# Kernel tuning notes

Hardware: AMD Instinct MI355X
Metric: run time of the kernel (lower is better)

Reference implementation:

```python
import math
import jax, jax.numpy as jnp
import numpy as np

D_MODEL = 1024
N_HEADS = 16
HEAD_DIM = D_MODEL // N_HEADS
WINDOW = 1024
BATCH = 2
SEQ = 2048


def _alibi_slopes(n_heads):
    # power-of-2 branch of ALiBiPositionalEmbedding._get_slopes
    start = 2 ** (-2 ** (-(math.log2(n_heads) - 3)))
    return jnp.asarray([start * start ** i for i in range(n_heads)], dtype=jnp.float32)


def setup_inputs() -> dict:
    key = jax.random.key(0)
    ks = jax.random.split(key, 5)
    scale = 0.02
    return {
        "x": jax.random.normal(ks[0], (BATCH, SEQ, D_MODEL), dtype=jnp.float32),
        "wq": jax.random.normal(ks[1], (D_MODEL, D_MODEL), dtype=jnp.float32) * scale,
        "bq": jnp.zeros((D_MODEL,), dtype=jnp.float32),
        "wk": jax.random.normal(ks[2], (D_MODEL, D_MODEL), dtype=jnp.float32) * scale,
        "bk": jnp.zeros((D_MODEL,), dtype=jnp.float32),
        "wv": jax.random.normal(ks[3], (D_MODEL, D_MODEL), dtype=jnp.float32) * scale,
        "bv": jnp.zeros((D_MODEL,), dtype=jnp.float32),
        "wo": jax.random.normal(ks[4], (D_MODEL, D_MODEL), dtype=jnp.float32) * scale,
        "bo": jnp.zeros((D_MODEL,), dtype=jnp.float32),
    }


def reference(x, wq, bq, wk, bk, wv, bv, wo, bo):
    B, S, _ = x.shape
    # projections (torch Linear: y = x @ W.T + b)
    q = (x @ wq.T + bq).reshape(B, S, N_HEADS, HEAD_DIM).transpose(0, 2, 1, 3)
    k = (x @ wk.T + bk).reshape(B, S, N_HEADS, HEAD_DIM).transpose(0, 2, 1, 3)
    v = (x @ wv.T + bv).reshape(B, S, N_HEADS, HEAD_DIM).transpose(0, 2, 1, 3)

    scores = jnp.einsum("bhqd,bhkd->bhqk", q, k) / math.sqrt(HEAD_DIM)

    # ALiBi bias: -|i-j| * slope_h, shape [H, S, S]
    pos = jnp.arange(S)
    slopes = _alibi_slopes(N_HEADS)  # [H]
    pos_diff = -jnp.abs(pos[None, :] - pos[:, None]).astype(scores.dtype)  # [S,S]
    scores = scores + pos_diff[None, None, :, :] * slopes[None, :, None, None]

    # causal + sliding-window mask: allow row-WINDOW < col <= row
    row = pos[:, None]
    col = pos[None, :]
    mask = (col > row) | (col <= row - WINDOW)  # [S,S] True = masked out
    neg = jnp.finfo(scores.dtype).min
    scores = jnp.where(mask[None, None, :, :], neg, scores)

    probs = jax.nn.softmax(scores, axis=-1)
    out = jnp.einsum("bhqk,bhkd->bhqd", probs, v)  # [B,H,S,D]
    out = out.transpose(0, 2, 1, 3).reshape(B, S, D_MODEL)
    return out @ wo.T + bo
```

## Files before the change

kernel.cpp:

```cpp
#include <hip/hip_runtime.h>
#include <cstdint>
#include <cstddef>

#define S_LEN 2048
#define NH 16
#define HD 64
#define DM 1024
#define WIN 1024

typedef unsigned short u16;
typedef __attribute__((ext_vector_type(8))) short bf16x8;
typedef __attribute__((ext_vector_type(4))) short bf16x4;
typedef __attribute__((ext_vector_type(4))) float f32x4;
typedef __attribute__((ext_vector_type(4))) u16 u16x4;
typedef __attribute__((ext_vector_type(2))) uint32_t u32x2;
typedef __attribute__((ext_vector_type(4))) uint32_t u32x4;

__device__ inline u16 f2b(float f) {
  union { float f; uint32_t u; } x; x.f = f;
  uint32_t r = x.u + 0x7FFFu + ((x.u >> 16) & 1u);
  return (u16)(r >> 16);
}

__device__ inline uint32_t cvt_pk_bf16(float a, float b) {
  uint32_t r;
  asm("v_cvt_pk_bf16_f32 %0, %1, %2" : "=v"(r) : "v"(a), "v"(b));
  return r;
}

__device__ inline void gload16(const void* g, void* l) {
  __builtin_amdgcn_global_load_lds((const __attribute__((address_space(1))) void*)g,
                                   (__attribute__((address_space(3))) void*)l, 16, 0, 0);
}

__global__ __launch_bounds__(256) void cvt_kernel(const float* __restrict__ src,
                                                  u16* __restrict__ dst, int n) {
  int i = (blockIdx.x * 256 + threadIdx.x) * 4;
  if (i >= n) return;
  f32x4 v = *(const f32x4*)(src + i);
  u16x4 o;
  o[0] = f2b(v[0]); o[1] = f2b(v[1]); o[2] = f2b(v[2]); o[3] = f2b(v[3]);
  *(u16x4*)(dst + i) = o;
}

__global__ __launch_bounds__(256)
void cvt4_kernel(const float* __restrict__ a, const float* __restrict__ b,
                 const float* __restrict__ c, const float* __restrict__ d,
                 u16* __restrict__ oa, u16* __restrict__ ob,
                 u16* __restrict__ oc, u16* __restrict__ od) {
  const float* src; u16* dst;
  switch (blockIdx.y) {
    case 0: src = a; dst = oa; break;
    case 1: src = b; dst = ob; break;
    case 2: src = c; dst = oc; break;
    default: src = d; dst = od; break;
  }
  int i = (blockIdx.x * 256 + threadIdx.x) * 4;
  f32x4 v = *(const f32x4*)(src + i);
  u16x4 o;
  o[0] = f2b(v[0]); o[1] = f2b(v[1]); o[2] = f2b(v[2]); o[3] = f2b(v[3]);
  *(u16x4*)(dst + i) = o;
}

template<int EPI>
__global__ __launch_bounds__(256, 4)
void gemm_nt(const u16* __restrict__ A, const u16* __restrict__ B,
             const float* __restrict__ b0, const float* __restrict__ b1,
             const float* __restrict__ b2,
             float* __restrict__ outF, u16* __restrict__ outQ,
             int M, int N, int K) {
  __shared__ u16 As[128 * 32];
  __shared__ u16 Bs[128 * 32];
  const int t = threadIdx.x;
  const int lane = t & 63, wid = t >> 6;
  const int l15 = lane & 15, l4 = lane >> 4;
  const int wr = wid >> 1, wc = wid & 1;
  const int bmB = M >> 7, bnB = N >> 7;
  const int stripe = bmB >> 3;
  const int per = stripe * bnB;
  const int job = (blockIdx.x & 7) * per + (blockIdx.x >> 3);
  const int r_ = job % per;
  const int bm = ((job / per) * stripe + r_ / bnB) << 7;
  const int bn = (r_ % bnB) << 7;
  const int srow = wid * 16 + (lane >> 2), scol = (lane & 3) * 8;
  const u16* Ag = A + (size_t)(bm + srow) * K + scol;
  const u16* Bg = B + (size_t)(bn + srow) * K + scol;
  u16* As0 = As + wid * 512;
  u16* As1 = As + 2048 + wid * 512;
  u16* Bs0 = Bs + wid * 512;
  u16* Bs1 = Bs + 2048 + wid * 512;
  const size_t rstep = (size_t)64 * K;
  f32x4 acc[4][4];
#pragma unroll
  for (int i = 0; i < 4; i++)
#pragma unroll
    for (int j = 0; j < 4; j++) acc[i][j] = (f32x4){0.f, 0.f, 0.f, 0.f};

  for (int kb = 0; kb < K; kb += 32) {
    __syncthreads();
    gload16(Ag + kb, As0);
    gload16(Ag + kb + rstep, As1);
    gload16(Bg + kb, Bs0);
    gload16(Bg + kb + rstep, Bs1);
    __syncthreads();
    bf16x8 af[4], bq[4];
#pragma unroll
    for (int mi = 0; mi < 4; mi++)
      af[mi] = *(bf16x8*)&As[(wr * 64 + mi * 16 + l15) * 32 + l4 * 8];
#pragma unroll
    for (int ni = 0; ni < 4; ni++)
      bq[ni] = *(bf16x8*)&Bs[(wc * 64 + ni * 16 + l15) * 32 + l4 * 8];
#pragma unroll
    for (int mi = 0; mi < 4; mi++)
#pragma unroll
      for (int ni = 0; ni < 4; ni++)
        acc[mi][ni] = __builtin_amdgcn_mfma_f32_16x16x32_bf16(af[mi], bq[ni], acc[mi][ni], 0, 0, 0);
  }

  const int cb = bn >> 10;
  const float* bp = (EPI == 0) ? b0 : (cb == 0 ? b0 : (cb == 1 ? b1 : b2));
#pragma unroll
  for (int mi = 0; mi < 4; mi++) {
#pragma unroll
    for (int ni = 0; ni < 4; ni++) {
#pragma unroll
      for (int r = 0; r < 4; r++) {
        int row = bm + wr * 64 + mi * 16 + l4 * 4 + r;
        int col = bn + wc * 64 + ni * 16 + l15;
        float v = acc[mi][ni][r] + bp[col & (DM - 1)];
        if (EPI == 0) {
          outF[(size_t)row * N + col] = v;
        } else {
          int b = row >> 11, s = row & (S_LEN - 1);
          int which = col >> 10, cw = col & (DM - 1);
          int h = cw >> 6, d = cw & (HD - 1);
          outQ[(size_t)which * 4194304 +
               (((size_t)(b * NH + h)) * S_LEN + s) * HD + d] = f2b(v);
        }
      }
    }
  }
}

__global__ __launch_bounds__(256)
void transpose_v(const u16* __restrict__ V, u16* __restrict__ Vt) {
  const int bh = blockIdx.y;
  const int s0 = blockIdx.x * 64;
  __shared__ u16 tile[64][72];
  const int t = threadIdx.x;
  const u16* src = V + ((size_t)bh * S_LEN + s0) * HD;
#pragma unroll
  for (int i = 0; i < 2; i++) {
    int e = t * 8 + i * 2048;
    int r = e >> 6, c = e & 63;
    *(bf16x8*)&tile[r][c] = *(const bf16x8*)(src + e);
  }
  __syncthreads();
  u16* dst = Vt + (size_t)bh * HD * S_LEN + s0;
#pragma unroll
  for (int i = 0; i < 2; i++) {
    int e = t * 8 + i * 2048;
    int d = e >> 6, s = e & 63;
    bf16x8 tmp;
#pragma unroll
    for (int j = 0; j < 8; j++) tmp[j] = (short)tile[s + j][d];
    *(bf16x8*)&dst[(size_t)d * S_LEN + s] = tmp;
  }
}

__device__ __forceinline__ void stage_tiles(const char* __restrict__ Kg,
                                            const char* __restrict__ Vg,
                                            u16* __restrict__ Kl, u16* __restrict__ Vl,
                                            int t) {
#pragma unroll
  for (int shot = 0; shot < 2; shot++) {
    int o = shot * 4096 + t * 16;
    int sw = ((o >> 7) & 7) << 4;
    gload16(Kg + (o ^ sw), (char*)Kl + o);
    gload16(Vg + (size_t)(o >> 7) * 4096 + ((o & 127) ^ sw), (char*)Vl + o);
  }
}

__device__ __forceinline__ void process_tile16(
    int kb, const u16* __restrict__ Kl, const u16* __restrict__ Vl,
    const bf16x8 qf[2], const float c16[16],
    int qw, int l15, int hi, float slope2, float qks,
    float& lsum, f32x4 O[4]) {
  const int x = l15 & 7;
  f32x4 st[4];
#pragma unroll
  for (int f = 0; f < 4; f++) st[f] = (f32x4){0.f, 0.f, 0.f, 0.f};
#pragma unroll
  for (int ks = 0; ks < 2; ks++)
#pragma unroll
    for (int f = 0; f < 4; f++) {
      bf16x8 kf = *(const bf16x8*)&Kl[(16 * f + l15) * 64 + (((4 * ks + hi) ^ x) << 3)];
      st[f] = __builtin_amdgcn_mfma_f32_16x16x32_bf16(kf, qf[ks], st[f], 0, 0, 0);
    }

  const int dkb = kb + 4 * hi - (qw + l15);
  const float base = slope2 * (float)dkb - 8.f;
  const bool interior = (kb + 63 <= qw) && (kb - (qw + 15) > -WIN);
  float p[16];
  if (interior) {
#pragma unroll
    for (int f = 0; f < 4; f++)
#pragma unroll
      for (int r = 0; r < 4; r++)
        p[4 * f + r] = fmaf(st[f][r], qks, base + c16[4 * f + r]);
  } else {
#pragma unroll
    for (int f = 0; f < 4; f++)
#pragma unroll
      for (int r = 0; r < 4; r++) {
        int dk = dkb + 16 * f + r;
        float s = fmaf(st[f][r], qks, base + c16[4 * f + r]);
        p[4 * f + r] = (dk > 0 || dk <= -WIN) ? -3e38f : s;
      }
  }

#pragma unroll
  for (int r = 0; r < 16; r++) p[r] = exp2f(p[r]);
  float a8[8];
#pragma unroll
  for (int r = 0; r < 8; r++) a8[r] = p[r] + p[r + 8];
#pragma unroll
  for (int r = 0; r < 4; r++) a8[r] += a8[r + 4];
  lsum += (a8[0] + a8[1]) + (a8[2] + a8[3]);

  bf16x8 pb[2];
#pragma unroll
  for (int kc = 0; kc < 2; kc++) {
    u32x4 w4;
    w4[0] = cvt_pk_bf16(p[8 * kc + 0], p[8 * kc + 1]);
    w4[1] = cvt_pk_bf16(p[8 * kc + 2], p[8 * kc + 3]);
    w4[2] = cvt_pk_bf16(p[8 * kc + 4], p[8 * kc + 5]);
    w4[3] = cvt_pk_bf16(p[8 * kc + 6], p[8 * kc + 7]);
    pb[kc] = __builtin_bit_cast(bf16x8, w4);
  }

#pragma unroll
  for (int d = 0; d < 4; d++) {
#pragma unroll
    for (int kc = 0; kc < 2; kc++) {
      const int row = (16 * d + l15) * 64;
      bf16x4 a = *(const bf16x4*)&Vl[row + (((4 * kc + (hi >> 1)) ^ x) << 3) + 4 * (hi & 1)];
      bf16x4 bql = *(const bf16x4*)&Vl[row + (((4 * kc + 2 + (hi >> 1)) ^ x) << 3) + 4 * (hi & 1)];
      bf16x8 vf;
      vf[0] = a[0]; vf[1] = a[1]; vf[2] = a[2]; vf[3] = a[3];
      vf[4] = bql[0]; vf[5] = bql[1]; vf[6] = bql[2]; vf[7] = bql[3];
      O[d] = __builtin_amdgcn_mfma_f32_16x16x32_bf16(vf, pb[kc], O[d], 0, 0, 0);
    }
  }
}

__global__ __launch_bounds__(256, 4)
void attn_kernel(const u16* __restrict__ Q, const u16* __restrict__ Kg,
                 const u16* __restrict__ Vt, u16* __restrict__ attn) {
  __shared__ __align__(16) u16 Klds[2][4096];
  __shared__ __align__(16) u16 Vlds[2][4096];
  const int bid = blockIdx.x;
  const int job = (bid & 7) * 128 + (bid >> 3);
  const int bh = job >> 5;
  const int qb = ((31 - (job & 31)) + (bh << 3)) & 31;
  const int b = bh >> 4, h = bh & 15;
  const int tid = threadIdx.x;
  const int wid = tid >> 6, lane = tid & 63;
  const int l15 = lane & 15, hi = lane >> 4;
  const int q0 = qb << 6;
  const int qw = q0 + 16 * wid;
  const u16* Qp = Q + (size_t)bh * (S_LEN * HD);
  const char* Kbase = (const char*)(Kg + (size_t)bh * (S_LEN * HD));
  const char* Vbase = (const char*)(Vt + (size_t)bh * (HD * S_LEN));

  bf16x8 qf[2];
#pragma unroll
  for (int ks = 0; ks < 2; ks++)
    qf[ks] = *(const bf16x8*)(Qp + (size_t)(qw + l15) * HD + 32 * ks + 8 * hi);

  const float slope2 = exp2f(-0.5f * (float)(h + 1)) * 1.44269504f;
  const float qks = 0.125f * 1.44269504f;
  float c16[16];
#pragma unroll
  for (int f = 0; f < 4; f++)
#pragma unroll
    for (int r = 0; r < 4; r++) c16[4 * f + r] = slope2 * (float)(16 * f + r);

  float lsum = 0.f;
  f32x4 O[4];
#pragma unroll
  for (int d = 0; d < 4; d++) O[d] = (f32x4){0.f, 0.f, 0.f, 0.f};

  int lo_u = q0 - (WIN - 1); if (lo_u < 0) lo_u = 0; lo_u &= ~63;
  const int hi_u = q0;
  int lo_w = qw - (WIN - 1); if (lo_w < 0) lo_w = 0; lo_w &= ~63;
  const int last_w = (qw + 15) & ~63;

  stage_tiles(Kbase + (size_t)lo_u * 128, Vbase + (size_t)lo_u * 2,
              Klds[0], Vlds[0], tid);
  int cur = 0;
  for (int kb = lo_u; kb <= hi_u; kb += 64) {
    __syncthreads();
    if (kb + 64 <= hi_u)
      stage_tiles(Kbase + (size_t)(kb + 64) * 128, Vbase + (size_t)(kb + 64) * 2,
                  Klds[cur ^ 1], Vlds[cur ^ 1], tid);
    if (kb >= lo_w && kb <= last_w)
      process_tile16(kb, Klds[cur], Vlds[cur], qf, c16,
                     qw, l15, hi, slope2, qks, lsum, O);
    cur ^= 1;
  }

  lsum += __shfl_xor(lsum, 16, 64);
  lsum += __shfl_xor(lsum, 32, 64);

  const float invl = 1.f / lsum;
  u16* op = attn + ((size_t)(b * S_LEN) + qw + l15) * DM + h * HD + 4 * hi;
#pragma unroll
  for (int d = 0; d < 4; d++) {
    u32x2 w;
    w[0] = cvt_pk_bf16(O[d][0] * invl, O[d][1] * invl);
    w[1] = cvt_pk_bf16(O[d][2] * invl, O[d][3] * invl);
    *(u32x2*)(op + d * 16) = w;
  }
}

extern "C" void kernel_launch(void* const* d_in, const int* in_sizes, int n_in,
                              void* d_out, int out_size, void* d_ws, size_t ws_size,
                              hipStream_t stream) {
  const float* x  = (const float*)d_in[0];
  const float* wq = (const float*)d_in[1];
  const float* bq = (const float*)d_in[2];
  const float* wk = (const float*)d_in[3];
  const float* bk = (const float*)d_in[4];
  const float* wv = (const float*)d_in[5];
  const float* bv = (const float*)d_in[6];
  const float* wo = (const float*)d_in[7];
  const float* bo = (const float*)d_in[8];

  char* ws = (char*)d_ws;
  u16* xb    = (u16*)(ws);
  u16* wqkvb = (u16*)(ws + 8388608);
  u16* wob   = (u16*)(ws + 14680064);
  u16* QKVb  = (u16*)(ws + 16777216);
  u16* Vtb   = (u16*)(ws + 41943040);
  u16* Ab    = (u16*)(ws + 50331648);
  u16* Vb    = QKVb + 2 * 4194304;

  const int M = 4096;

  cvt_kernel<<<dim3(4096), dim3(256), 0, stream>>>(x, xb, 4194304);
  cvt4_kernel<<<dim3(1024, 4), dim3(256), 0, stream>>>(
      wq, wk, wv, wo, wqkvb, wqkvb + 1048576, wqkvb + 2097152, wob);

  gemm_nt<1><<<dim3(768), dim3(256), 0, stream>>>(xb, wqkvb, bq, bk, bv,
                                                  nullptr, QKVb, M, 3072, DM);

  transpose_v<<<dim3(32, 32), dim3(256), 0, stream>>>(Vb, Vtb);

  attn_kernel<<<dim3(1024), dim3(256), 0, stream>>>(QKVb, QKVb + 4194304, Vtb, Ab);

  gemm_nt<0><<<dim3(256), dim3(256), 0, stream>>>(Ab, wob, bo, nullptr, nullptr,
                                                  (float*)d_out, nullptr, M, DM, DM);
}
```

Before: 114.1 us.

## Split attention key range across two blocks and merge partials in combine kernel

Each query block's key/value tile range is split into two halves handled by separate workgroups, doubling the attention grid. Each half writes unnormalized bf16 partial outputs and row sums into reused workspace buffers. A new combine kernel adds the two partials and divides by the summed row totals. The aim is better load balance and occupancy across CUs for the causal sliding-window workload. The cost is an extra launch, extra memory traffic for the partials, duplicated Q loads, and some precision loss from storing unnormalized partials in bf16.

```diff
diff --git a/kernel.cpp b/kernel.cpp
--- a/kernel.cpp
+++ b/kernel.cpp
@@ -20,6 +20,11 @@
   union { float f; uint32_t u; } x; x.f = f;
   uint32_t r = x.u + 0x7FFFu + ((x.u >> 16) & 1u);
   return (u16)(r >> 16);
+}
+
+__device__ inline float b2f(u16 v) {
+  union { uint32_t u; float f; } x; x.u = ((uint32_t)v) << 16;
+  return x.f;
 }
 
 __device__ inline uint32_t cvt_pk_bf16(float a, float b) {
@@ -256,13 +261,17 @@
 
 __global__ __launch_bounds__(256, 4)
 void attn_kernel(const u16* __restrict__ Q, const u16* __restrict__ Kg,
-                 const u16* __restrict__ Vt, u16* __restrict__ attn) {
+                 const u16* __restrict__ Vt,
+                 u16* __restrict__ PA, u16* __restrict__ PB,
+                 float* __restrict__ LA, float* __restrict__ LB) {
   __shared__ __align__(16) u16 Klds[2][4096];
   __shared__ __align__(16) u16 Vlds[2][4096];
   const int bid = blockIdx.x;
-  const int job = (bid & 7) * 128 + (bid >> 3);
-  const int bh = job >> 5;
-  const int qb = ((31 - (job & 31)) + (bh << 3)) & 31;
+  const int job = (bid & 7) * 256 + (bid >> 3);
+  const int bh = job >> 6;
+  const int rem = job & 63;
+  const int qb = ((31 - (rem >> 1)) + (bh << 3)) & 31;
+  const int half = rem & 1;
   const int b = bh >> 4, h = bh & 15;
   const int tid = threadIdx.x;
   const int wid = tid >> 6, lane = tid & 63;
@@ -291,37 +300,69 @@
 #pragma unroll
   for (int d = 0; d < 4; d++) O[d] = (f32x4){0.f, 0.f, 0.f, 0.f};
 
-  int lo_u = q0 - (WIN - 1); if (lo_u < 0) lo_u = 0; lo_u &= ~63;
-  const int hi_u = q0;
+  int LO = q0 - (WIN - 1); if (LO < 0) LO = 0; LO &= ~63;
+  const int HI = q0;
+  const int nt = ((HI - LO) >> 6) + 1;
+  const int nA = (nt + 1) >> 1;
+  const int t0 = half ? LO + nA * 64 : LO;
+  const int t1 = half ? HI : LO + (nA - 1) * 64;
   int lo_w = qw - (WIN - 1); if (lo_w < 0) lo_w = 0; lo_w &= ~63;
   const int last_w = (qw + 15) & ~63;
 
-  stage_tiles(Kbase + (size_t)lo_u * 128, Vbase + (size_t)lo_u * 2,
-              Klds[0], Vlds[0], tid);
-  int cur = 0;
-  for (int kb = lo_u; kb <= hi_u; kb += 64) {
-    __syncthreads();
-    if (kb + 64 <= hi_u)
-      stage_tiles(Kbase + (size_t)(kb + 64) * 128, Vbase + (size_t)(kb + 64) * 2,
-                  Klds[cur ^ 1], Vlds[cur ^ 1], tid);
-    if (kb >= lo_w && kb <= last_w)
-      process_tile16(kb, Klds[cur], Vlds[cur], qf, c16,
-                     qw, l15, hi, slope2, qks, lsum, O);
-    cur ^= 1;
+  if (t0 <= t1) {
+    stage_tiles(Kbase + (size_t)t0 * 128, Vbase + (size_t)t0 * 2,
+                Klds[0], Vlds[0], tid);
+    int cur = 0;
+    for (int kb = t0; kb <= t1; kb += 64) {
+      __syncthreads();
+      if (kb + 64 <= t1)
+        stage_tiles(Kbase + (size_t)(kb + 64) * 128, Vbase + (size_t)(kb + 64) * 2,
+                    Klds[cur ^ 1], Vlds[cur ^ 1], tid);
+      if (kb >= lo_w && kb <= last_w)
+        process_tile16(kb, Klds[cur], Vlds[cur], qf, c16,
+                       qw, l15, hi, slope2, qks, lsum, O);
+      cur ^= 1;
+    }
   }
 
   lsum += __shfl_xor(lsum, 16, 64);
   lsum += __shfl_xor(lsum, 32, 64);
 
-  const float invl = 1.f / lsum;
-  u16* op = attn + ((size_t)(b * S_LEN) + qw + l15) * DM + h * HD + 4 * hi;
+  u16* P = half ? PB : PA;
+  float* L = half ? LB : LA;
+  u16* op = P + ((size_t)(b * S_LEN) + qw + l15) * DM + h * HD + 4 * hi;
 #pragma unroll
   for (int d = 0; d < 4; d++) {
     u32x2 w;
-    w[0] = cvt_pk_bf16(O[d][0] * invl, O[d][1] * invl);
-    w[1] = cvt_pk_bf16(O[d][2] * invl, O[d][3] * invl);
+    w[0] = cvt_pk_bf16(O[d][0], O[d][1]);
+    w[1] = cvt_pk_bf16(O[d][2], O[d][3]);
     *(u32x2*)(op + d * 16) = w;
   }
+  if (hi == 0) L[(size_t)bh * S_LEN + qw + l15] = lsum;
+}
+
+__global__ __launch_bounds__(256)
+void combine_kernel(const u16* __restrict__ PA, const u16* __restrict__ PB,
+                    const float* __restrict__ LA, const float* __restrict__ LB,
+                    u16* __restrict__ out) {
+  const size_t e = ((size_t)blockIdx.x * 256 + threadIdx.x) * 8;
+  const int d0 = (int)(e & 1023);
+  const int srow = (int)(e >> 10);
+  const int b = srow >> 11, s = srow & (S_LEN - 1);
+  const int h = d0 >> 6;
+  const size_t li = ((size_t)(b * NH + h)) * S_LEN + s;
+  const float inv = 1.f / (LA[li] + LB[li]);
+  bf16x8 a = *(const bf16x8*)(PA + e);
+  bf16x8 c = *(const bf16x8*)(PB + e);
+  u16x4 o0, o1;
+#pragma unroll
+  for (int j = 0; j < 4; j++)
+    o0[j] = f2b((b2f((u16)a[j]) + b2f((u16)c[j])) * inv);
+#pragma unroll
+  for (int j = 0; j < 4; j++)
+    o1[j] = f2b((b2f((u16)a[4 + j]) + b2f((u16)c[4 + j])) * inv);
+  *(u16x4*)(out + e) = o0;
+  *(u16x4*)(out + e + 4) = o1;
 }
 
 extern "C" void kernel_launch(void* const* d_in, const int* in_sizes, int n_in,
@@ -339,11 +380,15 @@
 
   char* ws = (char*)d_ws;
   u16* xb    = (u16*)(ws);
+  u16* PB    = xb;
   u16* wqkvb = (u16*)(ws + 8388608);
+  float* LA  = (float*)(ws + 8388608);
+  float* LB  = (float*)(ws + 8912896);
   u16* wob   = (u16*)(ws + 14680064);
   u16* QKVb  = (u16*)(ws + 16777216);
   u16* Vtb   = (u16*)(ws + 41943040);
   u16* Ab    = (u16*)(ws + 50331648);
+  u16* PA    = Ab;
   u16* Vb    = QKVb + 2 * 4194304;
 
   const int M = 4096;
@@ -357,7 +402,10 @@
 
   transpose_v<<<dim3(32, 32), dim3(256), 0, stream>>>(Vb, Vtb);
 
-  attn_kernel<<<dim3(1024), dim3(256), 0, stream>>>(QKVb, QKVb + 4194304, Vtb, Ab);
+  attn_kernel<<<dim3(2048), dim3(256), 0, stream>>>(QKVb, QKVb + 4194304, Vtb,
+                                                    PA, PB, LA, LB);
+
+  combine_kernel<<<dim3(2048), dim3(256), 0, stream>>>(PA, PB, LA, LB, Ab);
 
   gemm_nt<0><<<dim3(256), dim3(256), 0, stream>>>(Ab, wob, bo, nullptr, nullptr,
                                                   (float*)d_out, nullptr, M, DM, DM);
```

New measurement: 119.6 us. 1.05x slower.

## Double GEMM K-tile to 64 with XOR-swizzled LDS and merge conversion kernels

Applied to the files above, without the earlier changes.

The bf16 GEMM now loads a 64-wide K slice per iteration instead of 32, which halves the number of barrier pairs. The LDS layout uses an XOR swizzle on 16-byte chunks to avoid bank conflicts on the wider rows. The two fp32-to-bf16 conversion launches are merged into one kernel to save a launch. LDS per block doubles to 32 KB, which could lower occupancy under the launch bound of 4 blocks per CU.

```diff
diff --git a/kernel.cpp b/kernel.cpp
--- a/kernel.cpp
+++ b/kernel.cpp
@@ -33,33 +33,30 @@
                                    (__attribute__((address_space(3))) void*)l, 16, 0, 0);
 }
 
-__global__ __launch_bounds__(256) void cvt_kernel(const float* __restrict__ src,
-                                                  u16* __restrict__ dst, int n) {
-  int i = (blockIdx.x * 256 + threadIdx.x) * 4;
-  if (i >= n) return;
-  f32x4 v = *(const f32x4*)(src + i);
+__global__ __launch_bounds__(256)
+void cvt_all(const float* __restrict__ x,
+             const float* __restrict__ wq, const float* __restrict__ wk,
+             const float* __restrict__ wv, const float* __restrict__ wo,
+             u16* __restrict__ xb, u16* __restrict__ wqkvb, u16* __restrict__ wob) {
+  size_t i = ((size_t)blockIdx.x * 256 + threadIdx.x) * 4;
+  const float* src; u16* dst;
+  if (i < 4194304) {
+    src = x + i; dst = xb + i;
+  } else {
+    size_t j = i - 4194304;
+    int w = (int)(j >> 20);
+    size_t off = j & 1048575;
+    switch (w) {
+      case 0:  src = wq + off; dst = wqkvb + off; break;
+      case 1:  src = wk + off; dst = wqkvb + 1048576 + off; break;
+      case 2:  src = wv + off; dst = wqkvb + 2097152 + off; break;
+      default: src = wo + off; dst = wob + off; break;
+    }
+  }
+  f32x4 v = *(const f32x4*)src;
   u16x4 o;
   o[0] = f2b(v[0]); o[1] = f2b(v[1]); o[2] = f2b(v[2]); o[3] = f2b(v[3]);
-  *(u16x4*)(dst + i) = o;
-}
-
-__global__ __launch_bounds__(256)
-void cvt4_kernel(const float* __restrict__ a, const float* __restrict__ b,
-                 const float* __restrict__ c, const float* __restrict__ d,
-                 u16* __restrict__ oa, u16* __restrict__ ob,
-                 u16* __restrict__ oc, u16* __restrict__ od) {
-  const float* src; u16* dst;
-  switch (blockIdx.y) {
-    case 0: src = a; dst = oa; break;
-    case 1: src = b; dst = ob; break;
-    case 2: src = c; dst = oc; break;
-    default: src = d; dst = od; break;
-  }
-  int i = (blockIdx.x * 256 + threadIdx.x) * 4;
-  f32x4 v = *(const f32x4*)(src + i);
-  u16x4 o;
-  o[0] = f2b(v[0]); o[1] = f2b(v[1]); o[2] = f2b(v[2]); o[3] = f2b(v[3]);
-  *(u16x4*)(dst + i) = o;
+  *(u16x4*)dst = o;
 }
 
 template<int EPI>
@@ -69,11 +66,12 @@
              const float* __restrict__ b2,
              float* __restrict__ outF, u16* __restrict__ outQ,
              int M, int N, int K) {
-  __shared__ u16 As[128 * 32];
-  __shared__ u16 Bs[128 * 32];
+  __shared__ u16 As[128 * 64];
+  __shared__ u16 Bs[128 * 64];
   const int t = threadIdx.x;
   const int lane = t & 63, wid = t >> 6;
   const int l15 = lane & 15, l4 = lane >> 4;
+  const int x = l15 & 7;
   const int wr = wid >> 1, wc = wid & 1;
   const int bmB = M >> 7, bnB = N >> 7;
   const int stripe = bmB >> 3;
@@ -82,39 +80,44 @@
   const int r_ = job % per;
   const int bm = ((job / per) * stripe + r_ / bnB) << 7;
   const int bn = (r_ % bnB) << 7;
-  const int srow = wid * 16 + (lane >> 2), scol = (lane & 3) * 8;
-  const u16* Ag = A + (size_t)(bm + srow) * K + scol;
-  const u16* Bg = B + (size_t)(bn + srow) * K + scol;
-  u16* As0 = As + wid * 512;
-  u16* As1 = As + 2048 + wid * 512;
-  u16* Bs0 = Bs + wid * 512;
-  u16* Bs1 = Bs + 2048 + wid * 512;
-  const size_t rstep = (size_t)64 * K;
+  const int srow0 = t >> 3;
+  const int colx = ((t * 16) & 127) ^ (((t >> 3) & 7) << 4);
+  const char* Ap = (const char*)A + ((size_t)(bm + srow0) * K) * 2 + colx;
+  const char* Bp = (const char*)B + ((size_t)(bn + srow0) * K) * 2 + colx;
+  const size_t sstr = (size_t)32 * K * 2;
+  char* Asd = (char*)As + t * 16;
+  char* Bsd = (char*)Bs + t * 16;
   f32x4 acc[4][4];
 #pragma unroll
   for (int i = 0; i < 4; i++)
 #pragma unroll
     for (int j = 0; j < 4; j++) acc[i][j] = (f32x4){0.f, 0.f, 0.f, 0.f};
 
-  for (int kb = 0; kb < K; kb += 32) {
+  for (int kb = 0; kb < K; kb += 64) {
     __syncthreads();
-    gload16(Ag + kb, As0);
-    gload16(Ag + kb + rstep, As1);
-    gload16(Bg + kb, Bs0);
-    gload16(Bg + kb + rstep, Bs1);
+#pragma unroll
+    for (int shot = 0; shot < 4; shot++) {
+      gload16(Ap + (size_t)kb * 2 + shot * sstr, Asd + shot * 4096);
+      gload16(Bp + (size_t)kb * 2 + shot * sstr, Bsd + shot * 4096);
+    }
     __syncthreads();
-    bf16x8 af[4], bq[4];
-#pragma unroll
-    for (int mi = 0; mi < 4; mi++)
-      af[mi] = *(bf16x8*)&As[(wr * 64 + mi * 16 + l15) * 32 + l4 * 8];
-#pragma unroll
-    for (int ni = 0; ni < 4; ni++)
-      bq[ni] = *(bf16x8*)&Bs[(wc * 64 + ni * 16 + l15) * 32 + l4 * 8];
-#pragma unroll
-    for (int mi = 0; mi < 4; mi++)
+#pragma unroll
+    for (int ks2 = 0; ks2 < 2; ks2++) {
+      bf16x8 af[4], bq[4];
+#pragma unroll
+      for (int mi = 0; mi < 4; mi++)
+        af[mi] = *(bf16x8*)&As[(wr * 64 + mi * 16 + l15) * 64 +
+                               (((ks2 * 4 + l4) ^ x) << 3)];
 #pragma unroll
       for (int ni = 0; ni < 4; ni++)
-        acc[mi][ni] = __builtin_amdgcn_mfma_f32_16x16x32_bf16(af[mi], bq[ni], acc[mi][ni], 0, 0, 0);
+        bq[ni] = *(bf16x8*)&Bs[(wc * 64 + ni * 16 + l15) * 64 +
+                               (((ks2 * 4 + l4) ^ x) << 3)];
+#pragma unroll
+      for (int mi = 0; mi < 4; mi++)
+#pragma unroll
+        for (int ni = 0; ni < 4; ni++)
+          acc[mi][ni] = __builtin_amdgcn_mfma_f32_16x16x32_bf16(af[mi], bq[ni], acc[mi][ni], 0, 0, 0);
+    }
   }
 
   const int cb = bn >> 10;
@@ -348,9 +351,8 @@
 
   const int M = 4096;
 
-  cvt_kernel<<<dim3(4096), dim3(256), 0, stream>>>(x, xb, 4194304);
-  cvt4_kernel<<<dim3(1024, 4), dim3(256), 0, stream>>>(
-      wq, wk, wv, wo, wqkvb, wqkvb + 1048576, wqkvb + 2097152, wob);
+  cvt_all<<<dim3(8192), dim3(256), 0, stream>>>(x, wq, wk, wv, wo,
+                                                xb, wqkvb, wob);
 
   gemm_nt<1><<<dim3(768), dim3(256), 0, stream>>>(xb, wqkvb, bq, bk, bv,
                                                   nullptr, QKVb, M, 3072, DM);
```

After: 107.5 us (median of 2 runs). 1.06x faster.
